# Performance work log

Measured on AMD Instinct MI355X. Metric: run time of the kernel, lower is better.

## Reference

```python
import jax, jax.numpy as jnp
import numpy as np

INPUT_DIM = 1024
OUTPUT_DIM = 1024
SPLINE_POINTS = 4

def setup_inputs() -> dict:
    key = jax.random.key(0)
    k1, k2 = jax.random.split(key)
    x = jax.random.normal(k1, (4096, INPUT_DIM), dtype=jnp.float32)
    spline_coeffs = jax.random.normal(k2, (OUTPUT_DIM, INPUT_DIM, SPLINE_POINTS, 4), dtype=jnp.float32)
    return {"x": x, "spline_coeffs": spline_coeffs}

def reference(x, spline_coeffs):
    # Per-feature min-max normalization over the batch dim (as in the torch code,
    # where x[:, j].min()/max() are taken over the batch).
    xmin = jnp.min(x, axis=0, keepdims=True)   # [1, D]
    xmax = jnp.max(x, axis=0, keepdims=True)
    xn = (x - xmin) / (xmax - xmin)            # [B, D]

    # The original sums the cubic polynomial over all spline_points, so the
    # effective coefficients are the sum over the spline_points axis.
    c = jnp.sum(spline_coeffs, axis=2)         # [O, D, 4]

    x2 = xn * xn
    x3 = x2 * xn
    # out[b, o] = sum_d c0*x^3 + c1*x^2 + c2*x + c3
    out = (jnp.einsum('bd,od->bo', x3, c[..., 0])
           + jnp.einsum('bd,od->bo', x2, c[..., 1])
           + jnp.einsum('bd,od->bo', xn, c[..., 2])
           + jnp.sum(c[..., 3], axis=1)[None, :])
    return out
```

## Files before the change

kernel.cpp:

```cpp
#include <hip/hip_runtime.h>
#include <hip/hip_bf16.h>
#include <stdint.h>
#include <stddef.h>

typedef __bf16 bf16;
typedef __attribute__((ext_vector_type(4))) __bf16 bf16x4;
typedef __attribute__((ext_vector_type(8))) __bf16 bf16x8;
typedef __attribute__((ext_vector_type(4))) float f32x4;

#define BATCH 4096
#define DIM 1024
#define ODIM 1024
#define K3 3072

#define WS_P      0
#define WS_PMIN   0
#define WS_PMAX   1048576
#define WS_CB     25165824
#define WS_BIAS   31457280
#define WS_MINV   31461376
#define WS_SCALE  31465472

#define ASYNC16(g, l)                                                          \
  __builtin_amdgcn_global_load_lds(                                            \
      (__attribute__((address_space(1))) void*)(g),                            \
      (__attribute__((address_space(3))) void*)(l), 16, 0, 0)

__global__ void k_minmax_part(const float* __restrict__ x,
                              float* __restrict__ pmin,
                              float* __restrict__ pmax) {
  const int t = threadIdx.x;
  const int ch = blockIdx.x;
  const float* p = x + (size_t)ch * 16 * DIM + (t << 2);
  f32x4 mn = {1e30f, 1e30f, 1e30f, 1e30f};
  f32x4 mx = {-1e30f, -1e30f, -1e30f, -1e30f};
#pragma unroll
  for (int r = 0; r < 16; ++r) {
    f32x4 v = *(const f32x4*)(p + (size_t)r * DIM);
#pragma unroll
    for (int j = 0; j < 4; ++j) {
      mn[j] = fminf(mn[j], v[j]);
      mx[j] = fmaxf(mx[j], v[j]);
    }
  }
  *(f32x4*)(pmin + ch * DIM + (t << 2)) = mn;
  *(f32x4*)(pmax + ch * DIM + (t << 2)) = mx;
}

__global__ void k_minmax_final(const float* __restrict__ pmin,
                               const float* __restrict__ pmax,
                               float* __restrict__ minv,
                               float* __restrict__ scale) {
  __shared__ float smn[16][17], smx[16][17];
  const int t = threadIdx.x;
  const int g = blockIdx.x;
  const int cl = t & 15;
  const int cs = t >> 4;
  const int col = g * 16 + cl;
  float mn = 1e30f, mx = -1e30f;
#pragma unroll
  for (int c = 0; c < 16; ++c) {
    int ch = cs * 16 + c;
    mn = fminf(mn, pmin[ch * DIM + col]);
    mx = fmaxf(mx, pmax[ch * DIM + col]);
  }
  smn[cs][cl] = mn;
  smx[cs][cl] = mx;
  __syncthreads();
  if (t < 16) {
    float m1 = smn[0][t], m2 = smx[0][t];
#pragma unroll
    for (int i = 1; i < 16; ++i) {
      m1 = fminf(m1, smn[i][t]);
      m2 = fmaxf(m2, smx[i][t]);
    }
    minv[g * 16 + t] = m1;
    scale[g * 16 + t] = 1.0f / (m2 - m1);
  }
}

__global__ void k_prep(const float* __restrict__ x,
                       const float* __restrict__ minv,
                       const float* __restrict__ scale,
                       bf16* __restrict__ P,
                       const float* __restrict__ sp,
                       bf16* __restrict__ CB,
                       float* __restrict__ bias) {
  __shared__ float red[4];
  const int t = threadIdx.x;
  if (blockIdx.x < 1024) {
    const int b0 = blockIdx.x << 2;
    const int d = t << 2;
    f32x4 mn = *(const f32x4*)(minv + d);
    f32x4 sc = *(const f32x4*)(scale + d);
#pragma unroll
    for (int i = 0; i < 4; ++i) {
      const int b = b0 + i;
      f32x4 xv = *(const f32x4*)(x + (size_t)b * DIM + d);
      bf16x4 o3, o2, o1;
#pragma unroll
      for (int j = 0; j < 4; ++j) {
        float xn = (xv[j] - mn[j]) * sc[j];
        float x2 = xn * xn;
        float x3 = x2 * xn;
        o3[j] = (bf16)x3;
        o2[j] = (bf16)x2;
        o1[j] = (bf16)xn;
      }
      size_t base = (size_t)b * K3 + d;
      *(bf16x4*)(P + base) = o3;
      *(bf16x4*)(P + base + 1024) = o2;
      *(bf16x4*)(P + base + 2048) = o1;
    }
  } else {
    const int o = blockIdx.x - 1024;
    const int d = t << 2;
    f32x4 s[4];
#pragma unroll
    for (int dd = 0; dd < 4; ++dd) {
      const float* p = sp + ((size_t)o * DIM + d + dd) * 16;
      f32x4 acc = *(const f32x4*)(p);
      acc += *(const f32x4*)(p + 4);
      acc += *(const f32x4*)(p + 8);
      acc += *(const f32x4*)(p + 12);
      s[dd] = acc;
    }
    size_t cb = (size_t)o * K3 + d;
    bf16x4 c0 = {(bf16)s[0][0], (bf16)s[1][0], (bf16)s[2][0], (bf16)s[3][0]};
    bf16x4 c1 = {(bf16)s[0][1], (bf16)s[1][1], (bf16)s[2][1], (bf16)s[3][1]};
    bf16x4 c2 = {(bf16)s[0][2], (bf16)s[1][2], (bf16)s[2][2], (bf16)s[3][2]};
    *(bf16x4*)(CB + cb) = c0;
    *(bf16x4*)(CB + cb + 1024) = c1;
    *(bf16x4*)(CB + cb + 2048) = c2;
    float v = s[0][3] + s[1][3] + s[2][3] + s[3][3];
#pragma unroll
    for (int off = 32; off > 0; off >>= 1) v += __shfl_down(v, off, 64);
    int lane = t & 63, w = t >> 6;
    if (lane == 0) red[w] = v;
    __syncthreads();
    if (t == 0) bias[o] = red[0] + red[1] + red[2] + red[3];
  }
}

#define BM 128
#define BN 128
#define BKE 64
#define NIT (K3 / BKE)
__global__ __launch_bounds__(256, 1) void k_gemm(const bf16* __restrict__ P,
                                                 const bf16* __restrict__ CBm,
                                                 const float* __restrict__ bias,
                                                 float* __restrict__ out) {
  __shared__ bf16 sA[BM * BKE];
  __shared__ bf16 sB[BN * BKE];

  const int tid = threadIdx.x;
  const int wave = tid >> 6;
  const int lane = tid & 63;
  const int bm = blockIdx.x * BM;
  const int bn = blockIdx.y * BN;
  const int wr = (wave >> 1) * 64;
  const int wc = (wave & 1) * 64;

  const size_t rowbytes = (size_t)K3 * 2;

  const char* gAp[4];
  const char* gBp[4];
  int ldso[4];
#pragma unroll
  for (int i = 0; i < 4; ++i) {
    int off = i * 4096 + tid * 16;
    int row = off >> 7;
    int q = (off >> 4) & 7;
    int gb = (q ^ (row & 7)) * 16;
    gAp[i] = (const char*)P + (size_t)(bm + row) * rowbytes + gb;
    gBp[i] = (const char*)CBm + (size_t)(bn + row) * rowbytes + gb;
    ldso[i] = i * 4096 + wave * 1024;
  }

  f32x4 acc[4][4] = {};

  const int mrow = lane & 15;
  const int kq = lane >> 4;

  for (int k0 = 0; k0 < K3; k0 += BKE) {
    const size_t kb = (size_t)k0 * 2;
#pragma unroll
    for (int i = 0; i < 4; ++i) ASYNC16(gAp[i] + kb, (char*)sA + ldso[i]);
#pragma unroll
    for (int i = 0; i < 4; ++i) ASYNC16(gBp[i] + kb, (char*)sB + ldso[i]);
    __syncthreads();

#pragma unroll
    for (int ks = 0; ks < 2; ++ks) {
      bf16x8 af[4], bg[4];
#pragma unroll
      for (int i = 0; i < 4; ++i) {
        int row = wr + i * 16 + mrow;
        int sq = (ks * 4 + kq) ^ (row & 7);
        af[i] = *(const bf16x8*)&sA[row * BKE + sq * 8];
      }
#pragma unroll
      for (int j = 0; j < 4; ++j) {
        int row = wc + j * 16 + mrow;
        int sq = (ks * 4 + kq) ^ (row & 7);
        bg[j] = *(const bf16x8*)&sB[row * BKE + sq * 8];
      }
#pragma unroll
      for (int i = 0; i < 4; ++i)
#pragma unroll
        for (int j = 0; j < 4; ++j)
          acc[i][j] = __builtin_amdgcn_mfma_f32_16x16x32_bf16(af[i], bg[j],
                                                              acc[i][j], 0, 0, 0);
    }
    __syncthreads();
  }

  const int ccol = lane & 15;
  const int crow = (lane >> 4) * 4;
#pragma unroll
  for (int j = 0; j < 4; ++j) {
    const int col = bn + wc + j * 16 + ccol;
    const float bv = bias[col];
#pragma unroll
    for (int i = 0; i < 4; ++i) {
      const int row0 = bm + wr + i * 16 + crow;
#pragma unroll
      for (int r = 0; r < 4; ++r)
        out[(size_t)(row0 + r) * ODIM + col] = acc[i][j][r] + bv;
    }
  }
}

extern "C" void kernel_launch(void* const* d_in, const int* in_sizes, int n_in,
                              void* d_out, int out_size, void* d_ws, size_t ws_size,
                              hipStream_t stream) {
  (void)in_sizes; (void)n_in; (void)out_size; (void)ws_size;
  const float* x = (const float*)d_in[0];
  const float* sp = (const float*)d_in[1];
  float* out = (float*)d_out;
  char* ws = (char*)d_ws;

  bf16* Pm = (bf16*)(ws + WS_P);
  bf16* CBm = (bf16*)(ws + WS_CB);
  float* bias = (float*)(ws + WS_BIAS);
  float* pmin = (float*)(ws + WS_PMIN);
  float* pmax = (float*)(ws + WS_PMAX);
  float* minv = (float*)(ws + WS_MINV);
  float* scale = (float*)(ws + WS_SCALE);

  k_minmax_part<<<256, 256, 0, stream>>>(x, pmin, pmax);
  k_minmax_final<<<64, 256, 0, stream>>>(pmin, pmax, minv, scale);
  k_prep<<<2048, 256, 0, stream>>>(x, minv, scale, Pm, sp, CBm, bias);
  k_gemm<<<dim3(32, 8), 256, 0, stream>>>(Pm, CBm, bias, out);
}
```

Before: 180.3 us.

## Fuse all stages into one persistent kernel with grid barriers and split-K GEMM

Merges min/max reduction, normalization/power prep, coefficient summation and the GEMM into a single 512-block persistent kernel, separated by atomic-counter grid barriers. The GEMM is split into two K halves so 512 blocks (two per CU) run it; the first half writes output plus bias, and after a barrier the second half adds its partial sum into the output. This removes three kernel launches and doubles GEMM occupancy, but adds grid-wide spin barriers, a read-modify-write pass over the output, and a deadlock risk if all 512 blocks cannot be resident at once.

```diff
diff --git a/kernel.cpp b/kernel.cpp
--- a/kernel.cpp
+++ b/kernel.cpp
@@ -12,95 +12,110 @@
 #define DIM 1024
 #define ODIM 1024
 #define K3 3072
+#define NB 512
 
 #define WS_P      0
 #define WS_PMIN   0
-#define WS_PMAX   1048576
+#define WS_PMAX   2097152
 #define WS_CB     25165824
 #define WS_BIAS   31457280
 #define WS_MINV   31461376
 #define WS_SCALE  31465472
+#define WS_SYNC   31469568
 
 #define ASYNC16(g, l)                                                          \
   __builtin_amdgcn_global_load_lds(                                            \
       (__attribute__((address_space(1))) void*)(g),                            \
       (__attribute__((address_space(3))) void*)(l), 16, 0, 0)
 
-__global__ void k_minmax_part(const float* __restrict__ x,
-                              float* __restrict__ pmin,
-                              float* __restrict__ pmax) {
+__device__ __forceinline__ void gsync(int* cnt) {
+  __syncthreads();
+  if (threadIdx.x == 0) {
+    __threadfence();
+    __hip_atomic_fetch_add(cnt, 1, __ATOMIC_RELEASE, __HIP_MEMORY_SCOPE_AGENT);
+    while (__hip_atomic_load(cnt, __ATOMIC_ACQUIRE, __HIP_MEMORY_SCOPE_AGENT) < NB)
+      __builtin_amdgcn_s_sleep(8);
+    __threadfence();
+  }
+  __syncthreads();
+}
+
+#define BM 128
+#define BN 128
+#define BKE 64
+#define NIT (1536 / BKE)
+
+__global__ __launch_bounds__(256, 2) void k_fused(
+    const float* __restrict__ x, const float* __restrict__ sp,
+    bf16* __restrict__ P, bf16* __restrict__ CB, float* __restrict__ bias,
+    float* __restrict__ pmin, float* __restrict__ pmax,
+    float* __restrict__ minv, float* __restrict__ scale,
+    int* __restrict__ sync, float* __restrict__ out) {
+  __shared__ bf16 sA[BM * BKE];
+  __shared__ bf16 sB[BN * BKE];
+  __shared__ float smn[16][17], smx[16][17];
+  __shared__ float red[4];
+
+  const int bid = blockIdx.x;
   const int t = threadIdx.x;
-  const int ch = blockIdx.x;
-  const float* p = x + (size_t)ch * 16 * DIM + (t << 2);
-  f32x4 mn = {1e30f, 1e30f, 1e30f, 1e30f};
-  f32x4 mx = {-1e30f, -1e30f, -1e30f, -1e30f};
-#pragma unroll
-  for (int r = 0; r < 16; ++r) {
-    f32x4 v = *(const f32x4*)(p + (size_t)r * DIM);
-#pragma unroll
-    for (int j = 0; j < 4; ++j) {
-      mn[j] = fminf(mn[j], v[j]);
-      mx[j] = fmaxf(mx[j], v[j]);
-    }
-  }
-  *(f32x4*)(pmin + ch * DIM + (t << 2)) = mn;
-  *(f32x4*)(pmax + ch * DIM + (t << 2)) = mx;
-}
-
-__global__ void k_minmax_final(const float* __restrict__ pmin,
-                               const float* __restrict__ pmax,
-                               float* __restrict__ minv,
-                               float* __restrict__ scale) {
-  __shared__ float smn[16][17], smx[16][17];
-  const int t = threadIdx.x;
-  const int g = blockIdx.x;
-  const int cl = t & 15;
-  const int cs = t >> 4;
-  const int col = g * 16 + cl;
-  float mn = 1e30f, mx = -1e30f;
-#pragma unroll
-  for (int c = 0; c < 16; ++c) {
-    int ch = cs * 16 + c;
-    mn = fminf(mn, pmin[ch * DIM + col]);
-    mx = fmaxf(mx, pmax[ch * DIM + col]);
-  }
-  smn[cs][cl] = mn;
-  smx[cs][cl] = mx;
-  __syncthreads();
-  if (t < 16) {
-    float m1 = smn[0][t], m2 = smx[0][t];
-#pragma unroll
-    for (int i = 1; i < 16; ++i) {
-      m1 = fminf(m1, smn[i][t]);
-      m2 = fmaxf(m2, smx[i][t]);
-    }
-    minv[g * 16 + t] = m1;
-    scale[g * 16 + t] = 1.0f / (m2 - m1);
-  }
-}
-
-__global__ void k_prep(const float* __restrict__ x,
-                       const float* __restrict__ minv,
-                       const float* __restrict__ scale,
-                       bf16* __restrict__ P,
-                       const float* __restrict__ sp,
-                       bf16* __restrict__ CB,
-                       float* __restrict__ bias) {
-  __shared__ float red[4];
-  const int t = threadIdx.x;
-  if (blockIdx.x < 1024) {
-    const int b0 = blockIdx.x << 2;
+
+  {
+    const float* xp = x + (size_t)bid * 8 * DIM + (t << 2);
+    f32x4 mn = {1e30f, 1e30f, 1e30f, 1e30f};
+    f32x4 mx = {-1e30f, -1e30f, -1e30f, -1e30f};
+#pragma unroll
+    for (int r = 0; r < 8; ++r) {
+      f32x4 v = *(const f32x4*)(xp + (size_t)r * DIM);
+#pragma unroll
+      for (int j = 0; j < 4; ++j) {
+        mn[j] = fminf(mn[j], v[j]);
+        mx[j] = fmaxf(mx[j], v[j]);
+      }
+    }
+    *(f32x4*)(pmin + bid * DIM + (t << 2)) = mn;
+    *(f32x4*)(pmax + bid * DIM + (t << 2)) = mx;
+  }
+  gsync(sync + 0);
+
+  if (bid < 64) {
+    const int cl = t & 15;
+    const int cs = t >> 4;
+    const int col = bid * 16 + cl;
+    float mn = 1e30f, mx = -1e30f;
+#pragma unroll 4
+    for (int c = 0; c < 32; ++c) {
+      int ch = cs * 32 + c;
+      mn = fminf(mn, pmin[ch * DIM + col]);
+      mx = fmaxf(mx, pmax[ch * DIM + col]);
+    }
+    smn[cs][cl] = mn;
+    smx[cs][cl] = mx;
+    __syncthreads();
+    if (t < 16) {
+      float m1 = smn[0][t], m2 = smx[0][t];
+#pragma unroll
+      for (int i = 1; i < 16; ++i) {
+        m1 = fminf(m1, smn[i][t]);
+        m2 = fmaxf(m2, smx[i][t]);
+      }
+      minv[bid * 16 + t] = m1;
+      scale[bid * 16 + t] = 1.0f / (m2 - m1);
+    }
+  }
+  gsync(sync + 1);
+
+  {
     const int d = t << 2;
-    f32x4 mn = *(const f32x4*)(minv + d);
-    f32x4 sc = *(const f32x4*)(scale + d);
-#pragma unroll
-    for (int i = 0; i < 4; ++i) {
-      const int b = b0 + i;
+    f32x4 mnv = *(const f32x4*)(minv + d);
+    f32x4 scv = *(const f32x4*)(scale + d);
+#pragma unroll
+    for (int r = 0; r < 8; ++r) {
+      const int b = bid * 8 + r;
       f32x4 xv = *(const f32x4*)(x + (size_t)b * DIM + d);
       bf16x4 o3, o2, o1;
 #pragma unroll
       for (int j = 0; j < 4; ++j) {
-        float xn = (xv[j] - mn[j]) * sc[j];
+        float xn = (xv[j] - mnv[j]) * scv[j];
         float x2 = xn * xn;
         float x3 = x2 * xn;
         o3[j] = (bf16)x3;
@@ -112,18 +127,20 @@
       *(bf16x4*)(P + base + 1024) = o2;
       *(bf16x4*)(P + base + 2048) = o1;
     }
-  } else {
-    const int o = blockIdx.x - 1024;
+  }
+#pragma unroll
+  for (int oo = 0; oo < 2; ++oo) {
+    const int o = bid * 2 + oo;
     const int d = t << 2;
     f32x4 s[4];
 #pragma unroll
     for (int dd = 0; dd < 4; ++dd) {
       const float* p = sp + ((size_t)o * DIM + d + dd) * 16;
-      f32x4 acc = *(const f32x4*)(p);
-      acc += *(const f32x4*)(p + 4);
-      acc += *(const f32x4*)(p + 8);
-      acc += *(const f32x4*)(p + 12);
-      s[dd] = acc;
+      f32x4 acc4 = *(const f32x4*)(p);
+      acc4 += *(const f32x4*)(p + 4);
+      acc4 += *(const f32x4*)(p + 8);
+      acc4 += *(const f32x4*)(p + 12);
+      s[dd] = acc4;
     }
     size_t cb = (size_t)o * K3 + d;
     bf16x4 c0 = {(bf16)s[0][0], (bf16)s[1][0], (bf16)s[2][0], (bf16)s[3][0]};
@@ -135,61 +152,49 @@
     float v = s[0][3] + s[1][3] + s[2][3] + s[3][3];
 #pragma unroll
     for (int off = 32; off > 0; off >>= 1) v += __shfl_down(v, off, 64);
-    int lane = t & 63, w = t >> 6;
-    if (lane == 0) red[w] = v;
+    if ((t & 63) == 0) red[t >> 6] = v;
     __syncthreads();
     if (t == 0) bias[o] = red[0] + red[1] + red[2] + red[3];
-  }
-}
-
-#define BM 128
-#define BN 128
-#define BKE 64
-#define NIT (K3 / BKE)
-__global__ __launch_bounds__(256, 1) void k_gemm(const bf16* __restrict__ P,
-                                                 const bf16* __restrict__ CBm,
-                                                 const float* __restrict__ bias,
-                                                 float* __restrict__ out) {
-  __shared__ bf16 sA[BM * BKE];
-  __shared__ bf16 sB[BN * BKE];
-
-  const int tid = threadIdx.x;
-  const int wave = tid >> 6;
-  const int lane = tid & 63;
-  const int bm = blockIdx.x * BM;
-  const int bn = blockIdx.y * BN;
+    __syncthreads();
+  }
+  gsync(sync + 2);
+
+  const int kz = bid >> 8;
+  const int tb = bid & 255;
+  const int bm = (tb >> 3) * BM;
+  const int bn = (tb & 7) * BN;
+  const int wave = t >> 6;
+  const int lane = t & 63;
   const int wr = (wave >> 1) * 64;
   const int wc = (wave & 1) * 64;
-
   const size_t rowbytes = (size_t)K3 * 2;
+  const size_t kzoff = (size_t)kz * 1536 * 2;
 
   const char* gAp[4];
   const char* gBp[4];
   int ldso[4];
 #pragma unroll
   for (int i = 0; i < 4; ++i) {
-    int off = i * 4096 + tid * 16;
+    int off = i * 4096 + t * 16;
     int row = off >> 7;
     int q = (off >> 4) & 7;
     int gb = (q ^ (row & 7)) * 16;
-    gAp[i] = (const char*)P + (size_t)(bm + row) * rowbytes + gb;
-    gBp[i] = (const char*)CBm + (size_t)(bn + row) * rowbytes + gb;
+    gAp[i] = (const char*)P + (size_t)(bm + row) * rowbytes + kzoff + gb;
+    gBp[i] = (const char*)CB + (size_t)(bn + row) * rowbytes + kzoff + gb;
     ldso[i] = i * 4096 + wave * 1024;
   }
 
   f32x4 acc[4][4] = {};
-
   const int mrow = lane & 15;
   const int kq = lane >> 4;
 
-  for (int k0 = 0; k0 < K3; k0 += BKE) {
-    const size_t kb = (size_t)k0 * 2;
+  for (int k0 = 0; k0 < NIT; ++k0) {
+    const size_t kb = (size_t)k0 * (BKE * 2);
 #pragma unroll
     for (int i = 0; i < 4; ++i) ASYNC16(gAp[i] + kb, (char*)sA + ldso[i]);
 #pragma unroll
     for (int i = 0; i < 4; ++i) ASYNC16(gBp[i] + kb, (char*)sB + ldso[i]);
     __syncthreads();
-
 #pragma unroll
     for (int ks = 0; ks < 2; ++ks) {
       bf16x8 af[4], bg[4];
@@ -217,16 +222,34 @@
 
   const int ccol = lane & 15;
   const int crow = (lane >> 4) * 4;
-#pragma unroll
-  for (int j = 0; j < 4; ++j) {
-    const int col = bn + wc + j * 16 + ccol;
-    const float bv = bias[col];
-#pragma unroll
-    for (int i = 0; i < 4; ++i) {
-      const int row0 = bm + wr + i * 16 + crow;
-#pragma unroll
-      for (int r = 0; r < 4; ++r)
-        out[(size_t)(row0 + r) * ODIM + col] = acc[i][j][r] + bv;
+  if (kz == 0) {
+#pragma unroll
+    for (int j = 0; j < 4; ++j) {
+      const int col = bn + wc + j * 16 + ccol;
+      const float bv = bias[col];
+#pragma unroll
+      for (int i = 0; i < 4; ++i) {
+        const int row0 = bm + wr + i * 16 + crow;
+#pragma unroll
+        for (int r = 0; r < 4; ++r)
+          out[(size_t)(row0 + r) * ODIM + col] = acc[i][j][r] + bv;
+      }
+    }
+  }
+  gsync(sync + 3);
+  if (kz == 1) {
+#pragma unroll
+    for (int j = 0; j < 4; ++j) {
+      const int col = bn + wc + j * 16 + ccol;
+#pragma unroll
+      for (int i = 0; i < 4; ++i) {
+        const int row0 = bm + wr + i * 16 + crow;
+#pragma unroll
+        for (int r = 0; r < 4; ++r) {
+          size_t idx = (size_t)(row0 + r) * ODIM + col;
+          out[idx] += acc[i][j][r];
+        }
+      }
     }
   }
 }
@@ -247,9 +270,9 @@
   float* pmax = (float*)(ws + WS_PMAX);
   float* minv = (float*)(ws + WS_MINV);
   float* scale = (float*)(ws + WS_SCALE);
-
-  k_minmax_part<<<256, 256, 0, stream>>>(x, pmin, pmax);
-  k_minmax_final<<<64, 256, 0, stream>>>(pmin, pmax, minv, scale);
-  k_prep<<<2048, 256, 0, stream>>>(x, minv, scale, Pm, sp, CBm, bias);
-  k_gemm<<<dim3(32, 8), 256, 0, stream>>>(Pm, CBm, bias, out);
+  int* sync = (int*)(ws + WS_SYNC);
+
+  hipMemsetAsync(sync, 0, 4 * sizeof(int), stream);
+  k_fused<<<NB, 256, 0, stream>>>(x, sp, Pm, CBm, bias, pmin, pmax, minv, scale,
+                                  sync, out);
 }
```

After: 477.1 us. 165% more time.

## Split-K GEMM with atomic accumulation and merge min-max reduction stages

Applied to the files above, without the earlier changes.

The GEMM's K dimension is split in two, giving 512 blocks instead of 256 so more of the CUs are busy, and each half accumulates into the output with atomic adds. The output is zeroed in the prep kernel, and only the first K-half adds the bias. The column min/max reduction is restructured into one partial kernel (8 chunks of 512 rows) whose final reduction is folded into the prep kernel, removing one launch. The cost is atomic traffic to the output, an extra full write to zero it, and min/max work repeated by every prep block.

```diff
diff --git a/kernel.cpp b/kernel.cpp
--- a/kernel.cpp
+++ b/kernel.cpp
@@ -14,93 +14,93 @@
 #define K3 3072
 
 #define WS_P      0
-#define WS_PMIN   0
-#define WS_PMAX   1048576
 #define WS_CB     25165824
 #define WS_BIAS   31457280
-#define WS_MINV   31461376
-#define WS_SCALE  31465472
+#define WS_PMIN   31461376
+#define WS_PMAX   31494144
 
 #define ASYNC16(g, l)                                                          \
   __builtin_amdgcn_global_load_lds(                                            \
       (__attribute__((address_space(1))) void*)(g),                            \
       (__attribute__((address_space(3))) void*)(l), 16, 0, 0)
 
-__global__ void k_minmax_part(const float* __restrict__ x,
-                              float* __restrict__ pmin,
-                              float* __restrict__ pmax) {
+__global__ __launch_bounds__(256) void k_part(const float* __restrict__ x,
+                                              float* __restrict__ pmin,
+                                              float* __restrict__ pmax) {
+  __shared__ f32x4 smn[32][8], smx[32][8];
   const int t = threadIdx.x;
-  const int ch = blockIdx.x;
-  const float* p = x + (size_t)ch * 16 * DIM + (t << 2);
+  const int ch = blockIdx.x >> 5;
+  const int cg = blockIdx.x & 31;
+  const int lc = (t & 7) * 4;
+  const int rl = t >> 3;
+
+  const float* xp = x + (size_t)(ch * 512 + rl) * DIM + cg * 32 + lc;
   f32x4 mn = {1e30f, 1e30f, 1e30f, 1e30f};
   f32x4 mx = {-1e30f, -1e30f, -1e30f, -1e30f};
-#pragma unroll
-  for (int r = 0; r < 16; ++r) {
-    f32x4 v = *(const f32x4*)(p + (size_t)r * DIM);
+#pragma unroll 4
+  for (int it = 0; it < 16; ++it) {
+    f32x4 v = *(const f32x4*)(xp + (size_t)it * 32 * DIM);
 #pragma unroll
     for (int j = 0; j < 4; ++j) {
       mn[j] = fminf(mn[j], v[j]);
       mx[j] = fmaxf(mx[j], v[j]);
     }
   }
-  *(f32x4*)(pmin + ch * DIM + (t << 2)) = mn;
-  *(f32x4*)(pmax + ch * DIM + (t << 2)) = mx;
-}
-
-__global__ void k_minmax_final(const float* __restrict__ pmin,
-                               const float* __restrict__ pmax,
-                               float* __restrict__ minv,
-                               float* __restrict__ scale) {
-  __shared__ float smn[16][17], smx[16][17];
-  const int t = threadIdx.x;
-  const int g = blockIdx.x;
-  const int cl = t & 15;
-  const int cs = t >> 4;
-  const int col = g * 16 + cl;
-  float mn = 1e30f, mx = -1e30f;
-#pragma unroll
-  for (int c = 0; c < 16; ++c) {
-    int ch = cs * 16 + c;
-    mn = fminf(mn, pmin[ch * DIM + col]);
-    mx = fmaxf(mx, pmax[ch * DIM + col]);
-  }
-  smn[cs][cl] = mn;
-  smx[cs][cl] = mx;
+  smn[rl][t & 7] = mn;
+  smx[rl][t & 7] = mx;
   __syncthreads();
-  if (t < 16) {
-    float m1 = smn[0][t], m2 = smx[0][t];
-#pragma unroll
-    for (int i = 1; i < 16; ++i) {
-      m1 = fminf(m1, smn[i][t]);
-      m2 = fmaxf(m2, smx[i][t]);
-    }
-    minv[g * 16 + t] = m1;
-    scale[g * 16 + t] = 1.0f / (m2 - m1);
-  }
-}
-
-__global__ void k_prep(const float* __restrict__ x,
-                       const float* __restrict__ minv,
-                       const float* __restrict__ scale,
-                       bf16* __restrict__ P,
-                       const float* __restrict__ sp,
-                       bf16* __restrict__ CB,
-                       float* __restrict__ bias) {
+  if (t < 8) {
+    f32x4 m1 = smn[0][t], m2 = smx[0][t];
+#pragma unroll
+    for (int i = 1; i < 32; ++i) {
+      f32x4 a = smn[i][t], b = smx[i][t];
+#pragma unroll
+      for (int j = 0; j < 4; ++j) {
+        m1[j] = fminf(m1[j], a[j]);
+        m2[j] = fmaxf(m2[j], b[j]);
+      }
+    }
+    *(f32x4*)(pmin + ch * DIM + cg * 32 + t * 4) = m1;
+    *(f32x4*)(pmax + ch * DIM + cg * 32 + t * 4) = m2;
+  }
+}
+
+__global__ __launch_bounds__(256) void k_prep(const float* __restrict__ x,
+                                              const float* __restrict__ pmin,
+                                              const float* __restrict__ pmax,
+                                              bf16* __restrict__ P,
+                                              const float* __restrict__ sp,
+                                              bf16* __restrict__ CB,
+                                              float* __restrict__ bias,
+                                              float* __restrict__ out) {
   __shared__ float red[4];
   const int t = threadIdx.x;
-  if (blockIdx.x < 1024) {
-    const int b0 = blockIdx.x << 2;
+  const int bid = blockIdx.x;
+  if (bid < 512) {
     const int d = t << 2;
-    f32x4 mn = *(const f32x4*)(minv + d);
-    f32x4 sc = *(const f32x4*)(scale + d);
-#pragma unroll
-    for (int i = 0; i < 4; ++i) {
-      const int b = b0 + i;
+    f32x4 mnv = *(const f32x4*)(pmin + d);
+    f32x4 mxv = *(const f32x4*)(pmax + d);
+#pragma unroll
+    for (int ch = 1; ch < 8; ++ch) {
+      f32x4 a = *(const f32x4*)(pmin + ch * DIM + d);
+      f32x4 b = *(const f32x4*)(pmax + ch * DIM + d);
+#pragma unroll
+      for (int j = 0; j < 4; ++j) {
+        mnv[j] = fminf(mnv[j], a[j]);
+        mxv[j] = fmaxf(mxv[j], b[j]);
+      }
+    }
+    f32x4 scv;
+#pragma unroll
+    for (int j = 0; j < 4; ++j) scv[j] = 1.0f / (mxv[j] - mnv[j]);
+#pragma unroll
+    for (int r = 0; r < 8; ++r) {
+      const int b = bid * 8 + r;
       f32x4 xv = *(const f32x4*)(x + (size_t)b * DIM + d);
       bf16x4 o3, o2, o1;
 #pragma unroll
       for (int j = 0; j < 4; ++j) {
-        float xn = (xv[j] - mn[j]) * sc[j];
+        float xn = (xv[j] - mnv[j]) * scv[j];
         float x2 = xn * xn;
         float x3 = x2 * xn;
         o3[j] = (bf16)x3;
@@ -112,41 +112,49 @@
       *(bf16x4*)(P + base + 1024) = o2;
       *(bf16x4*)(P + base + 2048) = o1;
     }
+    const f32x4 z = {0.f, 0.f, 0.f, 0.f};
+    float* op = out + (size_t)bid * 8 * ODIM + d;
+#pragma unroll
+    for (int r = 0; r < 8; ++r) *(f32x4*)(op + (size_t)r * ODIM) = z;
   } else {
-    const int o = blockIdx.x - 1024;
-    const int d = t << 2;
-    f32x4 s[4];
-#pragma unroll
-    for (int dd = 0; dd < 4; ++dd) {
-      const float* p = sp + ((size_t)o * DIM + d + dd) * 16;
-      f32x4 acc = *(const f32x4*)(p);
-      acc += *(const f32x4*)(p + 4);
-      acc += *(const f32x4*)(p + 8);
-      acc += *(const f32x4*)(p + 12);
-      s[dd] = acc;
-    }
-    size_t cb = (size_t)o * K3 + d;
-    bf16x4 c0 = {(bf16)s[0][0], (bf16)s[1][0], (bf16)s[2][0], (bf16)s[3][0]};
-    bf16x4 c1 = {(bf16)s[0][1], (bf16)s[1][1], (bf16)s[2][1], (bf16)s[3][1]};
-    bf16x4 c2 = {(bf16)s[0][2], (bf16)s[1][2], (bf16)s[2][2], (bf16)s[3][2]};
-    *(bf16x4*)(CB + cb) = c0;
-    *(bf16x4*)(CB + cb + 1024) = c1;
-    *(bf16x4*)(CB + cb + 2048) = c2;
-    float v = s[0][3] + s[1][3] + s[2][3] + s[3][3];
-#pragma unroll
-    for (int off = 32; off > 0; off >>= 1) v += __shfl_down(v, off, 64);
-    int lane = t & 63, w = t >> 6;
-    if (lane == 0) red[w] = v;
-    __syncthreads();
-    if (t == 0) bias[o] = red[0] + red[1] + red[2] + red[3];
+#pragma unroll
+    for (int oo = 0; oo < 2; ++oo) {
+      const int o = (bid - 512) * 2 + oo;
+      const int d = t << 2;
+      f32x4 s[4];
+#pragma unroll
+      for (int dd = 0; dd < 4; ++dd) {
+        const float* p = sp + ((size_t)o * DIM + d + dd) * 16;
+        f32x4 a = *(const f32x4*)(p);
+        a += *(const f32x4*)(p + 4);
+        a += *(const f32x4*)(p + 8);
+        a += *(const f32x4*)(p + 12);
+        s[dd] = a;
+      }
+      size_t cb = (size_t)o * K3 + d;
+      bf16x4 c0 = {(bf16)s[0][0], (bf16)s[1][0], (bf16)s[2][0], (bf16)s[3][0]};
+      bf16x4 c1 = {(bf16)s[0][1], (bf16)s[1][1], (bf16)s[2][1], (bf16)s[3][1]};
+      bf16x4 c2 = {(bf16)s[0][2], (bf16)s[1][2], (bf16)s[2][2], (bf16)s[3][2]};
+      *(bf16x4*)(CB + cb) = c0;
+      *(bf16x4*)(CB + cb + 1024) = c1;
+      *(bf16x4*)(CB + cb + 2048) = c2;
+      float v = s[0][3] + s[1][3] + s[2][3] + s[3][3];
+#pragma unroll
+      for (int off = 32; off > 0; off >>= 1) v += __shfl_down(v, off, 64);
+      if ((t & 63) == 0) red[t >> 6] = v;
+      __syncthreads();
+      if (t == 0) bias[o] = red[0] + red[1] + red[2] + red[3];
+      __syncthreads();
+    }
   }
 }
 
 #define BM 128
 #define BN 128
 #define BKE 64
-#define NIT (K3 / BKE)
-__global__ __launch_bounds__(256, 1) void k_gemm(const bf16* __restrict__ P,
+#define KHALF 1536
+#define NIT (KHALF / BKE)
+__global__ __launch_bounds__(256, 2) void k_gemm(const bf16* __restrict__ P,
                                                  const bf16* __restrict__ CBm,
                                                  const float* __restrict__ bias,
                                                  float* __restrict__ out) {
@@ -156,12 +164,16 @@
   const int tid = threadIdx.x;
   const int wave = tid >> 6;
   const int lane = tid & 63;
-  const int bm = blockIdx.x * BM;
-  const int bn = blockIdx.y * BN;
+  const int bid = blockIdx.x;
+  const int kz = bid >> 8;
+  const int tb = bid & 255;
+  const int bm = (tb >> 3) * BM;
+  const int bn = (tb & 7) * BN;
   const int wr = (wave >> 1) * 64;
   const int wc = (wave & 1) * 64;
 
   const size_t rowbytes = (size_t)K3 * 2;
+  const size_t kzoff = (size_t)kz * KHALF * 2;
 
   const char* gAp[4];
   const char* gBp[4];
@@ -172,24 +184,22 @@
     int row = off >> 7;
     int q = (off >> 4) & 7;
     int gb = (q ^ (row & 7)) * 16;
-    gAp[i] = (const char*)P + (size_t)(bm + row) * rowbytes + gb;
-    gBp[i] = (const char*)CBm + (size_t)(bn + row) * rowbytes + gb;
+    gAp[i] = (const char*)P + (size_t)(bm + row) * rowbytes + kzoff + gb;
+    gBp[i] = (const char*)CBm + (size_t)(bn + row) * rowbytes + kzoff + gb;
     ldso[i] = i * 4096 + wave * 1024;
   }
 
   f32x4 acc[4][4] = {};
-
   const int mrow = lane & 15;
   const int kq = lane >> 4;
 
-  for (int k0 = 0; k0 < K3; k0 += BKE) {
-    const size_t kb = (size_t)k0 * 2;
+  for (int k0 = 0; k0 < NIT; ++k0) {
+    const size_t kb = (size_t)k0 * (BKE * 2);
 #pragma unroll
     for (int i = 0; i < 4; ++i) ASYNC16(gAp[i] + kb, (char*)sA + ldso[i]);
 #pragma unroll
     for (int i = 0; i < 4; ++i) ASYNC16(gBp[i] + kb, (char*)sB + ldso[i]);
     __syncthreads();
-
 #pragma unroll
     for (int ks = 0; ks < 2; ++ks) {
       bf16x8 af[4], bg[4];
@@ -220,13 +230,14 @@
 #pragma unroll
   for (int j = 0; j < 4; ++j) {
     const int col = bn + wc + j * 16 + ccol;
-    const float bv = bias[col];
+    const float bv = (kz == 0) ? bias[col] : 0.0f;
 #pragma unroll
     for (int i = 0; i < 4; ++i) {
       const int row0 = bm + wr + i * 16 + crow;
 #pragma unroll
       for (int r = 0; r < 4; ++r)
-        out[(size_t)(row0 + r) * ODIM + col] = acc[i][j][r] + bv;
+        unsafeAtomicAdd(&out[(size_t)(row0 + r) * ODIM + col],
+                        acc[i][j][r] + bv);
     }
   }
 }
@@ -245,11 +256,8 @@
   float* bias = (float*)(ws + WS_BIAS);
   float* pmin = (float*)(ws + WS_PMIN);
   float* pmax = (float*)(ws + WS_PMAX);
-  float* minv = (float*)(ws + WS_MINV);
-  float* scale = (float*)(ws + WS_SCALE);
-
-  k_minmax_part<<<256, 256, 0, stream>>>(x, pmin, pmax);
-  k_minmax_final<<<64, 256, 0, stream>>>(pmin, pmax, minv, scale);
-  k_prep<<<2048, 256, 0, stream>>>(x, minv, scale, Pm, sp, CBm, bias);
-  k_gemm<<<dim3(32, 8), 256, 0, stream>>>(Pm, CBm, bias, out);
-}
+
+  k_part<<<256, 256, 0, stream>>>(x, pmin, pmax);
+  k_prep<<<1024, 256, 0, stream>>>(x, pmin, pmax, Pm, sp, CBm, bias, out);
+  k_gemm<<<512, 256, 0, stream>>>(Pm, CBm, bias, out);
+}
```

New measurement: 179.9 us. No clear change (-0.2%).
